# Kernel tuning notes

Measured on AMD Instinct MI355X. Metric: run time of the kernel, lower is better.

Reference implementation:

```python
import jax, jax.numpy as jnp
import numpy as np

B, D, H = 8192, 256, 1024


def setup_inputs() -> dict:
    key = jax.random.key(0)
    ks = jax.random.split(key, 24)
    glorot = lambda k, o, i: jax.random.uniform(k, (o, i), jnp.float32, -1.0, 1.0) * jnp.sqrt(6.0 / (o + i))
    inp = {
        'x': jax.random.normal(ks[0], (B, D), jnp.float32),
        'm': (jax.random.uniform(ks[1], (B, D)) < 0.8).astype(jnp.float32),  # binary observation mask
        'delta': jax.random.uniform(ks[2], (B, D), jnp.float32),             # nonnegative time gaps
        'h': jax.random.normal(ks[3], (B, H), jnp.float32),
        'x_last_obs': jax.random.normal(ks[4], (B, D), jnp.float32),
        'x_mean': jax.random.normal(ks[5], (D,), jnp.float32),
        'W_gamma_x': jax.random.uniform(ks[6], (D,), jnp.float32, 0.001, 0.01),
        'b_gamma_x': jnp.zeros((D,), jnp.float32),
        'W_gamma_h': glorot(ks[7], H, D), 'b_gamma_h': jnp.zeros((H,), jnp.float32),
        'W_xz': glorot(ks[8], H, D), 'W_hz': glorot(ks[9], H, H),
        'W_mz': glorot(ks[10], H, D), 'b_mz': jnp.zeros((H,), jnp.float32),
        'W_xr': glorot(ks[11], H, D), 'W_hr': glorot(ks[12], H, H),
        'W_mr': glorot(ks[13], H, D), 'b_mr': jnp.zeros((H,), jnp.float32),
        'W_xh': glorot(ks[14], H, D), 'W_hh': glorot(ks[15], H, H),
        'W_mh': glorot(ks[16], H, D), 'b_mh': jnp.zeros((H,), jnp.float32),
    }
    return inp


def reference(x, m, delta, h, x_last_obs, x_mean,
              W_gamma_x, b_gamma_x, W_gamma_h, b_gamma_h,
              W_xz, W_hz, W_mz, b_mz,
              W_xr, W_hr, W_mr, b_mr,
              W_xh, W_hh, W_mh, b_mh):
    # input decay (per-feature) and hidden decay (linear of delta)
    gamma_x = jnp.exp(-jax.nn.relu(delta * W_gamma_x + b_gamma_x))        # [B, D]
    gamma_h = jnp.exp(-jax.nn.relu(delta @ W_gamma_h.T + b_gamma_h))     # [B, H]
    # imputation
    x_last_obs_new = jnp.where(m > 0, x, x_last_obs)
    x_imputed = gamma_x * x_last_obs_new + (1.0 - gamma_x) * x_mean
    x_hat = m * x + (1.0 - m) * x_imputed
    h_decayed = gamma_h * h
    # GRU gates (eval mode: no recurrent dropout)
    z = jax.nn.sigmoid(x_hat @ W_xz.T + h_decayed @ W_hz.T + m @ W_mz.T + b_mz)
    r = jax.nn.sigmoid(x_hat @ W_xr.T + h_decayed @ W_hr.T + m @ W_mr.T + b_mr)
    h_tilde = jnp.tanh(x_hat @ W_xh.T + (r * h_decayed) @ W_hh.T + m @ W_mh.T + b_mh)
    h_new = (1.0 - z) * h_decayed + z * h_tilde
    return h_new, x_last_obs_new
```

## Files before the change

### kernel.cpp

```cpp
#include <hip/hip_runtime.h>
#include <cstdint>
#include <cstddef>

typedef unsigned short u16;
typedef __attribute__((ext_vector_type(8))) short s16x8;
typedef __attribute__((ext_vector_type(8))) u16 u16x8;
typedef __attribute__((ext_vector_type(4))) float f32x4;

#define DEV static __device__ __forceinline__
#define GPTR(p) (const __attribute__((address_space(1))) void*)(p)
#define LPTR(p) (__attribute__((address_space(3))) void*)(p)
#define BAR __builtin_amdgcn_s_barrier()
#define SETP1 __builtin_amdgcn_s_setprio(1)
#define SETP0 __builtin_amdgcn_s_setprio(0)

DEV float b2f(u16 u) { union { unsigned i; float f; } c; c.i = ((unsigned)u) << 16; return c.f; }
DEV u16 f2b(float f) {
  union { float f; unsigned i; } c; c.f = f;
  unsigned r = (c.i + 0x7fffu + ((c.i >> 16) & 1u)) >> 16;
  return (u16)r;
}
DEV float sigm(float x) { return 1.0f / (1.0f + __expf(-x)); }

__global__ __launch_bounds__(256) void pack_w(
    const float* __restrict__ Wxz, const float* __restrict__ Whz, const float* __restrict__ Wmz,
    const float* __restrict__ Wxr, const float* __restrict__ Whr, const float* __restrict__ Wmr,
    const float* __restrict__ Wxh, const float* __restrict__ Whh, const float* __restrict__ Wmh,
    const float* __restrict__ Wgh,
    u16* __restrict__ WZR, u16* __restrict__ WH, u16* __restrict__ WGH)
{
  int t = blockIdx.x * 256 + threadIdx.x;
  const float* src;
  u16* dst;
  if (t < 589824) {
    int row = t / 192;
    int col = (t % 192) * 8;
    int rr = row & 1023;
    const float *wx, *wh, *wm;
    if (row < 1024)      { wx = Wxz; wh = Whz; wm = Wmz; }
    else if (row < 2048) { wx = Wxr; wh = Whr; wm = Wmr; }
    else                 { wx = Wxh; wh = Whh; wm = Wmh; }
    if (col < 256)       src = wx + rr * 256 + col;
    else if (col < 1280) src = wh + (size_t)rr * 1024 + (col - 256);
    else                 src = wm + rr * 256 + (col - 1280);
    dst = (row < 2048) ? (WZR + (size_t)row * 1536 + col)
                       : (WH + (size_t)(row - 2048) * 1536 + col);
  } else {
    int t2 = t - 589824;
    src = Wgh + t2 * 8;
    dst = WGH + t2 * 8;
  }
  f32x4 a = *(const f32x4*)src;
  f32x4 b = *(const f32x4*)(src + 4);
  u16x8 v;
#pragma unroll
  for (int j = 0; j < 4; ++j) { v[j] = f2b(a[j]); v[j + 4] = f2b(b[j]); }
  *(u16x8*)dst = v;
}

__global__ __launch_bounds__(256) void elem_k(
    const float* __restrict__ x, const float* __restrict__ m, const float* __restrict__ delta,
    const float* __restrict__ xlo, const float* __restrict__ x_mean,
    const float* __restrict__ Wgx, const float* __restrict__ bgx,
    u16* __restrict__ X1, u16* __restrict__ X2, u16* __restrict__ Dbf,
    float* __restrict__ out_xlo)
{
  int t = blockIdx.x * 256 + threadIdx.x;
  int row = t >> 5;
  int col = (t & 31) * 8;
  size_t base = (size_t)row * 256 + col;
  u16x8 vxhat, vm16, vd16;
  f32x4 vlnew[2];
#pragma unroll
  for (int half = 0; half < 2; ++half) {
    f32x4 vx = *(const f32x4*)(x + base + half * 4);
    f32x4 vm = *(const f32x4*)(m + base + half * 4);
    f32x4 vd = *(const f32x4*)(delta + base + half * 4);
    f32x4 vl = *(const f32x4*)(xlo + base + half * 4);
    f32x4 vmean = *(const f32x4*)(x_mean + col + half * 4);
    f32x4 vwg = *(const f32x4*)(Wgx + col + half * 4);
    f32x4 vbg = *(const f32x4*)(bgx + col + half * 4);
#pragma unroll
    for (int j = 0; j < 4; ++j) {
      float mf = vm[j];
      float lnew = (mf > 0.5f) ? vx[j] : vl[j];
      vlnew[half][j] = lnew;
      float gx = __expf(-fmaxf(vd[j] * vwg[j] + vbg[j], 0.0f));
      float ximp = gx * lnew + (1.0f - gx) * vmean[j];
      float xhat = mf * vx[j] + (1.0f - mf) * ximp;
      vxhat[half * 4 + j] = f2b(xhat);
      vm16[half * 4 + j] = f2b(mf);
      vd16[half * 4 + j] = f2b(vd[j]);
    }
  }
  size_t r1536 = (size_t)row * 1536;
  *(u16x8*)(X1 + r1536 + col) = vxhat;
  *(u16x8*)(X2 + r1536 + col) = vxhat;
  *(u16x8*)(X1 + r1536 + 1280 + col) = vm16;
  *(u16x8*)(X2 + r1536 + 1280 + col) = vm16;
  *(u16x8*)(Dbf + base) = vd16;
  *(f32x4*)(out_xlo + base) = vlnew[0];
  *(f32x4*)(out_xlo + base + 4) = vlnew[1];
}

template<int EPI, int KK, int GXL>
__global__ __launch_bounds__(512, 4) void gemm256(
    const u16* __restrict__ A, const u16* __restrict__ W,
    const float* __restrict__ bias0, const float* __restrict__ bias1,
    const float* __restrict__ auxf,
    const u16* __restrict__ auxb,
    const u16* __restrict__ aux2b,
    u16* __restrict__ out0b,
    u16* __restrict__ out1b,
    float* __restrict__ outf)
{
  constexpr int P = KK / 32;
  constexpr int GX = 1 << GXL;
  __shared__ alignas(16) u16 As[3][8192];
  __shared__ alignas(16) u16 Bs[3][4096];

  const int tid = threadIdx.x, lane = tid & 63, wave = tid >> 6;
  const int wr = wave >> 1, wc = wave & 1;
  const int d = blockIdx.x;
  const int q = (int)gridDim.x >> 3;
  const int L = (d & 7) * q + (d >> 3);
  const int brow = (L >> GXL) * 256, bcol = (L & (GX - 1)) * 128;
  const int lr = lane & 15, g4 = lane >> 4;
  const int rc = (g4 ^ ((lr >> 1) & 3)) * 8;
  const int srow = tid >> 2;
  const int scs = ((tid & 3) ^ ((srow >> 1) & 3)) * 8;

  f32x4 acc[4][4];
#pragma unroll
  for (int i = 0; i < 4; ++i)
#pragma unroll
    for (int j = 0; j < 4; ++j) { f32x4 z0 = {0.f, 0.f, 0.f, 0.f}; acc[i][j] = z0; }

  const u16* aP = A + (size_t)(brow + srow) * KK + scs;
  const u16* aQ = aP + (size_t)128 * KK;
  const u16* bP = W + (size_t)(bcol + srow) * KK + scs;
  u16* dA = &As[0][0] + tid * 8;
  u16* dB = &Bs[0][0] + tid * 8;
  const u16* rA = &As[0][0] + (wr * 64 + lr) * 32 + rc;
  const u16* rB = &Bs[0][0] + (wc * 64 + lr) * 32 + rc;

  auto STAGE = [&](int slot, int ko) {
    __builtin_amdgcn_global_load_lds(GPTR(aP + ko), LPTR(dA + slot * 8192), 16, 0, 0);
    __builtin_amdgcn_global_load_lds(GPTR(aQ + ko), LPTR(dA + slot * 8192 + 4096), 16, 0, 0);
    __builtin_amdgcn_global_load_lds(GPTR(bP + ko), LPTR(dB + slot * 4096), 16, 0, 0);
  };

  STAGE(0, 0);
  STAGE(1, 32);
  asm volatile("s_waitcnt vmcnt(3)" ::: "memory");
  BAR;
  asm volatile("" ::: "memory");

#pragma unroll
  for (int u = 0; u < P; ++u) {
    const int sR = u % 3;
    const int sS = (u + 2) % 3;
    const int ko = ((u + 2 < P) ? (u + 2) : (P - 1)) * 32;
    STAGE(sS, ko);
    s16x8 af[4], bf[4];
#pragma unroll
    for (int i = 0; i < 4; ++i) af[i] = *(const s16x8*)(rA + sR * 8192 + i * 512);
#pragma unroll
    for (int j = 0; j < 4; ++j) bf[j] = *(const s16x8*)(rB + sR * 4096 + j * 512);
    SETP1;
#pragma unroll
    for (int i = 0; i < 4; ++i)
#pragma unroll
      for (int j = 0; j < 4; ++j)
        acc[i][j] = __builtin_amdgcn_mfma_f32_16x16x32_bf16(af[i], bf[j], acc[i][j], 0, 0, 0);
    SETP0;
    asm volatile("s_waitcnt vmcnt(3) lgkmcnt(0)" ::: "memory");
    BAR;
    asm volatile("" ::: "memory");
  }
  asm volatile("s_waitcnt vmcnt(0)" ::: "memory");

  const int row0 = brow + wr * 64 + g4 * 4;
  const int col0 = bcol + wc * 64 + lr;
#pragma unroll
  for (int i = 0; i < 4; ++i) {
#pragma unroll
    for (int j = 0; j < 4; ++j) {
      int c_ = col0 + j * 16;
#pragma unroll
      for (int qq = 0; qq < 4; ++qq) {
        int r_ = row0 + i * 16 + qq;
        float v = acc[i][j][qq];
        if constexpr (EPI == 0) {
          float p = v + bias0[c_];
          float gh = __expf(-fmaxf(p, 0.0f));
          float hd = gh * auxf[(size_t)r_ * 1024 + c_];
          out0b[(size_t)r_ * 1536 + 256 + c_] = f2b(hd);
        } else if constexpr (EPI == 1) {
          if (c_ < 1024) {
            out0b[(size_t)r_ * 1024 + c_] = f2b(sigm(v + bias0[c_]));
          } else {
            int jc = c_ - 1024;
            float rg = sigm(v + bias1[jc]);
            float hd = b2f(auxb[(size_t)r_ * 1536 + 256 + jc]);
            out1b[(size_t)r_ * 1536 + 256 + jc] = f2b(rg * hd);
          }
        } else {
          float ht = tanhf(v + bias0[c_]);
          float zz = b2f(aux2b[(size_t)r_ * 1024 + c_]);
          float hd = b2f(auxb[(size_t)r_ * 1536 + 256 + c_]);
          outf[(size_t)r_ * 1024 + c_] = (1.0f - zz) * hd + zz * ht;
        }
      }
    }
  }
}

extern "C" void kernel_launch(void* const* d_in, const int* in_sizes, int n_in,
                              void* d_out, int out_size, void* d_ws, size_t ws_size,
                              hipStream_t stream)
{
  const float* x     = (const float*)d_in[0];
  const float* m     = (const float*)d_in[1];
  const float* delta = (const float*)d_in[2];
  const float* h     = (const float*)d_in[3];
  const float* xlo   = (const float*)d_in[4];
  const float* xmean = (const float*)d_in[5];
  const float* Wgx   = (const float*)d_in[6];
  const float* bgx   = (const float*)d_in[7];
  const float* Wgh   = (const float*)d_in[8];
  const float* bgh   = (const float*)d_in[9];
  const float* Wxz   = (const float*)d_in[10];
  const float* Whz   = (const float*)d_in[11];
  const float* Wmz   = (const float*)d_in[12];
  const float* bmz   = (const float*)d_in[13];
  const float* Wxr   = (const float*)d_in[14];
  const float* Whr   = (const float*)d_in[15];
  const float* Wmr   = (const float*)d_in[16];
  const float* bmr   = (const float*)d_in[17];
  const float* Wxh   = (const float*)d_in[18];
  const float* Whh   = (const float*)d_in[19];
  const float* Wmh   = (const float*)d_in[20];
  const float* bmh   = (const float*)d_in[21];

  u16* X1  = (u16*)d_ws;
  u16* X2  = X1 + (size_t)8192 * 1536;
  u16* Z   = X2 + (size_t)8192 * 1536;
  u16* WZR = Z  + (size_t)8192 * 1024;
  u16* WH  = WZR + (size_t)2048 * 1536;
  u16* Dbf = WH + (size_t)1024 * 1536;
  u16* WGH = Dbf + (size_t)8192 * 256;

  float* out_h   = (float*)d_out;
  float* out_xlo = out_h + (size_t)8192 * 1024;

  pack_w<<<2432, 256, 0, stream>>>(Wxz, Whz, Wmz, Wxr, Whr, Wmr, Wxh, Whh, Wmh, Wgh, WZR, WH, WGH);
  elem_k<<<1024, 256, 0, stream>>>(x, m, delta, xlo, xmean, Wgx, bgx, X1, X2, Dbf, out_xlo);
  gemm256<0, 256, 3><<<256, 512, 0, stream>>>(
      Dbf, WGH, bgh, nullptr, h, nullptr, nullptr, X1, nullptr, nullptr);
  gemm256<1, 1536, 4><<<512, 512, 0, stream>>>(
      X1, WZR, bmz, bmr, nullptr, X1, nullptr, Z, X2, nullptr);
  gemm256<2, 1536, 3><<<256, 512, 0, stream>>>(
      X2, WH, bmh, nullptr, nullptr, X1, Z, nullptr, nullptr, out_h);
}
```

Measured before the change: 163.5 us.

## Enlarge GEMM tile to 256x256 with ping-pong LDS schedule

After: 212.8 us. 1.3x slower.

```diff
diff --git a/kernel.cpp b/kernel.cpp
--- a/kernel.cpp
+++ b/kernel.cpp
@@ -10,9 +10,12 @@
 #define DEV static __device__ __forceinline__
 #define GPTR(p) (const __attribute__((address_space(1))) void*)(p)
 #define LPTR(p) (__attribute__((address_space(3))) void*)(p)
+#define SCHEDB __builtin_amdgcn_sched_barrier(0)
 #define BAR __builtin_amdgcn_s_barrier()
 #define SETP1 __builtin_amdgcn_s_setprio(1)
 #define SETP0 __builtin_amdgcn_s_setprio(0)
+#define LGKM0 asm volatile("s_waitcnt lgkmcnt(0)" ::: "memory")
+#define VM4   asm volatile("s_waitcnt vmcnt(4)" ::: "memory")
 
 DEV float b2f(u16 u) { union { unsigned i; float f; } c; c.i = ((unsigned)u) << 16; return c.f; }
 DEV u16 f2b(float f) {
@@ -104,7 +107,7 @@
 }
 
 template<int EPI, int KK, int GXL>
-__global__ __launch_bounds__(512, 4) void gemm256(
+__global__ __launch_bounds__(512, 2) void gemm256(
     const u16* __restrict__ A, const u16* __restrict__ W,
     const float* __restrict__ bias0, const float* __restrict__ bias1,
     const float* __restrict__ auxf,
@@ -114,76 +117,117 @@
     u16* __restrict__ out1b,
     float* __restrict__ outf)
 {
-  constexpr int P = KK / 32;
+  constexpr int NT = KK / 64;
   constexpr int GX = 1 << GXL;
-  __shared__ alignas(16) u16 As[3][8192];
-  __shared__ alignas(16) u16 Bs[3][4096];
+  __shared__ alignas(16) u16 As[4][8192];
+  __shared__ alignas(16) u16 Bs[4][8192];
 
   const int tid = threadIdx.x, lane = tid & 63, wave = tid >> 6;
-  const int wr = wave >> 1, wc = wave & 1;
+  const int wr = wave >> 2, wc = wave & 3;
   const int d = blockIdx.x;
   const int q = (int)gridDim.x >> 3;
   const int L = (d & 7) * q + (d >> 3);
-  const int brow = (L >> GXL) * 256, bcol = (L & (GX - 1)) * 128;
+  const int brow = (L >> GXL) * 256, bcol = (L & (GX - 1)) * 256;
   const int lr = lane & 15, g4 = lane >> 4;
   const int rc = (g4 ^ ((lr >> 1) & 3)) * 8;
   const int srow = tid >> 2;
   const int scs = ((tid & 3) ^ ((srow >> 1) & 3)) * 8;
 
-  f32x4 acc[4][4];
-#pragma unroll
-  for (int i = 0; i < 4; ++i)
+  f32x4 acc[8][4];
+#pragma unroll
+  for (int i = 0; i < 8; ++i)
 #pragma unroll
     for (int j = 0; j < 4; ++j) { f32x4 z0 = {0.f, 0.f, 0.f, 0.f}; acc[i][j] = z0; }
 
   const u16* aP = A + (size_t)(brow + srow) * KK + scs;
   const u16* aQ = aP + (size_t)128 * KK;
   const u16* bP = W + (size_t)(bcol + srow) * KK + scs;
+  const u16* bQ = bP + (size_t)128 * KK;
   u16* dA = &As[0][0] + tid * 8;
   u16* dB = &Bs[0][0] + tid * 8;
-  const u16* rA = &As[0][0] + (wr * 64 + lr) * 32 + rc;
-  const u16* rB = &Bs[0][0] + (wc * 64 + lr) * 32 + rc;
-
-  auto STAGE = [&](int slot, int ko) {
-    __builtin_amdgcn_global_load_lds(GPTR(aP + ko), LPTR(dA + slot * 8192), 16, 0, 0);
-    __builtin_amdgcn_global_load_lds(GPTR(aQ + ko), LPTR(dA + slot * 8192 + 4096), 16, 0, 0);
-    __builtin_amdgcn_global_load_lds(GPTR(bP + ko), LPTR(dB + slot * 4096), 16, 0, 0);
+  const u16* rA = &As[0][0] + lr * 32 + rc;
+  const u16* rB = &Bs[0][0] + lr * 32 + rc;
+
+  auto SA = [&](int so, int ko) {
+    __builtin_amdgcn_global_load_lds(GPTR(aP + ko), LPTR(dA + so), 16, 0, 0);
+    __builtin_amdgcn_global_load_lds(GPTR(aQ + ko), LPTR(dA + so + 4096), 16, 0, 0);
   };
-
-  STAGE(0, 0);
-  STAGE(1, 32);
-  asm volatile("s_waitcnt vmcnt(3)" ::: "memory");
-  BAR;
-  asm volatile("" ::: "memory");
-
-#pragma unroll
-  for (int u = 0; u < P; ++u) {
-    const int sR = u % 3;
-    const int sS = (u + 2) % 3;
-    const int ko = ((u + 2 < P) ? (u + 2) : (P - 1)) * 32;
-    STAGE(sS, ko);
+  auto SB = [&](int so, int ko) {
+    __builtin_amdgcn_global_load_lds(GPTR(bP + ko), LPTR(dB + so), 16, 0, 0);
+    __builtin_amdgcn_global_load_lds(GPTR(bQ + ko), LPTR(dB + so + 4096), 16, 0, 0);
+  };
+
+  auto TILE = [&](int b, int ko) {
+    const int ro = b * 16384;
+    const int so = (b ^ 1) * 16384;
     s16x8 af[4], bf[4];
 #pragma unroll
-    for (int i = 0; i < 4; ++i) af[i] = *(const s16x8*)(rA + sR * 8192 + i * 512);
-#pragma unroll
-    for (int j = 0; j < 4; ++j) bf[j] = *(const s16x8*)(rB + sR * 4096 + j * 512);
+    for (int j = 0; j < 4; ++j) bf[j] = *(const s16x8*)(rB + ro + (wc * 64 + j * 16) * 32);
+#pragma unroll
+    for (int i = 0; i < 4; ++i) af[i] = *(const s16x8*)(rA + ro + (wr * 128 + i * 16) * 32);
+    SA(so, ko);
+    SCHEDB; BAR; LGKM0; SCHEDB;
     SETP1;
 #pragma unroll
     for (int i = 0; i < 4; ++i)
 #pragma unroll
       for (int j = 0; j < 4; ++j)
         acc[i][j] = __builtin_amdgcn_mfma_f32_16x16x32_bf16(af[i], bf[j], acc[i][j], 0, 0, 0);
-    SETP0;
-    asm volatile("s_waitcnt vmcnt(3) lgkmcnt(0)" ::: "memory");
-    BAR;
-    asm volatile("" ::: "memory");
+    SETP0; BAR;
+#pragma unroll
+    for (int i = 0; i < 4; ++i) af[i] = *(const s16x8*)(rA + ro + (wr * 128 + 64 + i * 16) * 32);
+    SB(so, ko);
+    SCHEDB; VM4; BAR; LGKM0; SCHEDB;
+    SETP1;
+#pragma unroll
+    for (int i = 0; i < 4; ++i)
+#pragma unroll
+      for (int j = 0; j < 4; ++j)
+        acc[4 + i][j] = __builtin_amdgcn_mfma_f32_16x16x32_bf16(af[i], bf[j], acc[4 + i][j], 0, 0, 0);
+    SETP0; BAR;
+#pragma unroll
+    for (int j = 0; j < 4; ++j) bf[j] = *(const s16x8*)(rB + ro + 8192 + (wc * 64 + j * 16) * 32);
+#pragma unroll
+    for (int i = 0; i < 4; ++i) af[i] = *(const s16x8*)(rA + ro + 8192 + (wr * 128 + i * 16) * 32);
+    SA(so + 8192, ko + 32);
+    SCHEDB; BAR; LGKM0; SCHEDB;
+    SETP1;
+#pragma unroll
+    for (int i = 0; i < 4; ++i)
+#pragma unroll
+      for (int j = 0; j < 4; ++j)
+        acc[i][j] = __builtin_amdgcn_mfma_f32_16x16x32_bf16(af[i], bf[j], acc[i][j], 0, 0, 0);
+    SETP0; BAR;
+#pragma unroll
+    for (int i = 0; i < 4; ++i) af[i] = *(const s16x8*)(rA + ro + 8192 + (wr * 128 + 64 + i * 16) * 32);
+    SB(so + 8192, ko + 32);
+    SCHEDB; VM4; BAR; LGKM0; SCHEDB;
+    SETP1;
+#pragma unroll
+    for (int i = 0; i < 4; ++i)
+#pragma unroll
+      for (int j = 0; j < 4; ++j)
+        acc[4 + i][j] = __builtin_amdgcn_mfma_f32_16x16x32_bf16(af[i], bf[j], acc[4 + i][j], 0, 0, 0);
+    SETP0; BAR;
+  };
+
+  SA(0, 0);    SB(0, 0);
+  SA(8192, 32); SB(8192, 32);
+  VM4; BAR;
+
+  for (int t = 0; t < NT - 2; t += 2) {
+    TILE(0, 64);
+    TILE(1, 128);
+    aP += 128; aQ += 128; bP += 128; bQ += 128;
   }
+  TILE(0, 64);
+  TILE(1, 0);
   asm volatile("s_waitcnt vmcnt(0)" ::: "memory");
 
-  const int row0 = brow + wr * 64 + g4 * 4;
+  const int row0 = brow + wr * 128 + g4 * 4;
   const int col0 = bcol + wc * 64 + lr;
 #pragma unroll
-  for (int i = 0; i < 4; ++i) {
+  for (int i = 0; i < 8; ++i) {
 #pragma unroll
     for (int j = 0; j < 4; ++j) {
       int c_ = col0 + j * 16;
@@ -256,10 +300,10 @@
 
   pack_w<<<2432, 256, 0, stream>>>(Wxz, Whz, Wmz, Wxr, Whr, Wmr, Wxh, Whh, Wmh, Wgh, WZR, WH, WGH);
   elem_k<<<1024, 256, 0, stream>>>(x, m, delta, xlo, xmean, Wgx, bgx, X1, X2, Dbf, out_xlo);
-  gemm256<0, 256, 3><<<256, 512, 0, stream>>>(
+  gemm256<0, 256, 2><<<128, 512, 0, stream>>>(
       Dbf, WGH, bgh, nullptr, h, nullptr, nullptr, X1, nullptr, nullptr);
-  gemm256<1, 1536, 4><<<512, 512, 0, stream>>>(
+  gemm256<1, 1536, 3><<<256, 512, 0, stream>>>(
       X1, WZR, bmz, bmr, nullptr, X1, nullptr, Z, X2, nullptr);
-  gemm256<2, 1536, 3><<<256, 512, 0, stream>>>(
+  gemm256<2, 1536, 2><<<128, 512, 0, stream>>>(
       X2, WH, bmh, nullptr, nullptr, X1, Z, nullptr, nullptr, out_h);
 }
```
